# Optimization experiments

Hardware: AMD Instinct MI355X
Metric: run time of the kernel (lower is better)

The kernel has to match this reference:

```python
import jax, jax.numpy as jnp
import numpy as np
import math

DIM = 4096
N_HEADS = 32
HEAD_DIM = DIM // N_HEADS  # 128
SEQLEN = 2048


def setup_inputs() -> dict:
    key = jax.random.key(0)
    ks = jax.random.split(key, 8)
    x = jax.random.normal(ks[0], (1, SEQLEN, DIM), dtype=jnp.float32)
    # freqs_cis as real view: (seqlen, head_dim//2, 2) = (cos, sin) of rotary angles
    theta = 10000.0 ** (-jnp.arange(0, HEAD_DIM, 2, dtype=jnp.float32) / HEAD_DIM)
    angles = jnp.arange(SEQLEN, dtype=jnp.float32)[:, None] * theta[None, :]
    freqs = jnp.stack([jnp.cos(angles), jnp.sin(angles)], axis=-1)  # (S, 64, 2)
    # causal additive mask (use -1e9 instead of -inf for numeric safety)
    mask = jnp.triu(jnp.full((SEQLEN, SEQLEN), -1e9, dtype=jnp.float32), k=1)[None, None]
    scale = 1.0 / math.sqrt(DIM)
    wq = jax.random.normal(ks[1], (DIM, DIM), dtype=jnp.float32) * scale
    wk = jax.random.normal(ks[2], (DIM, DIM), dtype=jnp.float32) * scale
    wv = jax.random.normal(ks[3], (DIM, DIM), dtype=jnp.float32) * scale
    wo = jax.random.normal(ks[4], (DIM, DIM), dtype=jnp.float32) * scale
    return {"x": x, "start_pos": 0, "freqs": freqs, "mask": mask,
            "wq": wq, "wk": wk, "wv": wv, "wo": wo}


def _rotary(xq, xk, freqs, seqlen, n_heads, head_dim):
    # Faithful to source: note the repo's slice(0, 2) means xq_ == xq (no pair swap).
    ll = freqs[:, :, 0:1]  # (S, hd/2, 1) cos
    rr = freqs[:, :, 1:2]  # (S, hd/2, 1) sin
    fl = jnp.concatenate([ll, ll], axis=-1).reshape(seqlen, 1, head_dim)
    fr = jnp.concatenate([-rr, rr], axis=-1).reshape(seqlen, 1, head_dim)
    xq_ = xq.reshape(seqlen, n_heads, head_dim // 2, 2).reshape(seqlen, n_heads, head_dim)  # == xq
    xk_ = xk.reshape(seqlen, n_heads, head_dim // 2, 2).reshape(seqlen, n_heads, head_dim)  # == xk
    return xq * fl + xq_ * fr, xk * fl + xk_ * fr


def reference(x, start_pos, freqs, mask, wq, wk, wv, wo):
    bsz, seqlen, dim = x.shape  # bsz == 1 (source squeezes batch)
    xs = x[0]  # (S, D) -- HE encrypt/linear/decrypt roundtrip == plain linear
    xq = xs @ wq.T
    xk = xs @ wk.T
    xv = xs @ wv.T
    xq = xq.reshape(seqlen, N_HEADS, HEAD_DIM)
    xk = xk.reshape(seqlen, N_HEADS, HEAD_DIM)
    xv = xv.reshape(seqlen, N_HEADS, HEAD_DIM)
    xq, xk = _rotary(xq, xk, freqs, seqlen, N_HEADS, HEAD_DIM)
    # start_pos == 0 and zero-initialized cache => keys/values are just xk/xv
    q = jnp.transpose(xq, (1, 0, 2))  # (H, S, Dh)
    k = jnp.transpose(xk, (1, 0, 2))
    v = jnp.transpose(xv, (1, 0, 2))
    scores = jnp.einsum('hqd,hkd->hqk', q, k) / math.sqrt(HEAD_DIM)  # (H, S, S)
    scores = scores[None] + mask  # (1, H, S, S)
    probs = jax.nn.softmax(scores, axis=-1)
    out = jnp.einsum('bhqk,hkd->bhqd', probs, v)  # (1, H, S, Dh)
    out = jnp.transpose(out, (0, 2, 1, 3)).reshape(bsz, seqlen, dim)
    return out @ wo.T
```

## Files before the change

### kernel.cpp

```cpp
#include <hip/hip_runtime.h>

#define DIM 4096
#define SEQ 2048
#define NH 32
#define HD 128

typedef __bf16 bf16x8 __attribute__((ext_vector_type(8)));
typedef float f32x4 __attribute__((ext_vector_type(4)));

#define QSCALE 0.12751649736765598f

__device__ inline ushort f2bf(float f) {
    union { float f; unsigned u; } v; v.f = f;
    unsigned r = v.u + 0x7fffu + ((v.u >> 16) & 1u);
    return (ushort)(r >> 16);
}

__global__ void conv_all(const float* __restrict__ x,  const float* __restrict__ wq,
                         const float* __restrict__ wk, const float* __restrict__ wv,
                         const float* __restrict__ wo,
                         ushort* __restrict__ xb,  ushort* __restrict__ wqb,
                         ushort* __restrict__ wkb, ushort* __restrict__ wvb,
                         ushort* __restrict__ wob) {
    int i = blockIdx.x * 256 + threadIdx.x;
    const float* src; ushort* dst; int off;
    const int n4x = (SEQ * DIM) / 4;
    if (i < n4x) { src = x; dst = xb; off = i; }
    else {
        int j = i - n4x;
        int w = j >> 22;
        off = j & ((1 << 22) - 1);
        src = (w == 0) ? wq : (w == 1) ? wk : (w == 2) ? wv : wo;
        dst = (w == 0) ? wqb : (w == 1) ? wkb : (w == 2) ? wvb : wob;
    }
    float4 v = ((const float4*)src)[off];
    ushort4 o;
    o.x = f2bf(v.x); o.y = f2bf(v.y); o.z = f2bf(v.z); o.w = f2bf(v.w);
    ((ushort4*)dst)[off] = o;
}

__global__ __launch_bounds__(256)
void gemm_qkv(const ushort* __restrict__ A,
              const ushort* __restrict__ Bq, const ushort* __restrict__ Bk,
              const ushort* __restrict__ Bv,
              ushort* __restrict__ qout, ushort* __restrict__ kout,
              ushort* __restrict__ vt, const float* __restrict__ freqs) {
    __shared__ __align__(16) ushort sA[128 * 64];
    __shared__ __align__(16) ushort sB[128 * 64];
    const int bi = blockIdx.x;
    const int x = bi & 7;
    const int l = bi >> 3;
    const int mblk = l & 15;
    const int nblk = x * 12 + (l >> 4);
    const int wsel = nblk >> 5;
    const int nloc = (nblk & 31) * 128;
    const int m0 = mblk * 128;
    const int tid = threadIdx.x;
    const int wave = tid >> 6, lane = tid & 63;
    const int quad = lane >> 4, c = lane & 15;
    const int wm = (wave >> 1) * 64, wn = (wave & 1) * 64;
    const ushort* B = (wsel == 0) ? Bq : (wsel == 1) ? Bk : Bv;
    const int K = DIM;

    const f32x4 vzero = {0.f, 0.f, 0.f, 0.f};
    f32x4 acc[4][4];
#pragma unroll
    for (int i = 0; i < 4; i++)
#pragma unroll
        for (int j = 0; j < 4; j++) acc[i][j] = vzero;

    const int srow8 = lane >> 3;
    const int sg    = (lane & 7) ^ srow8;
    const int scol  = sg * 8;
    const int rp0 = ((0 * 4 + quad) ^ (c & 7)) * 8;
    const int rp1 = ((1 * 4 + quad) ^ (c & 7)) * 8;
    const size_t arow0 = (size_t)(m0 + wave * 32) * K;
    const size_t brow0 = (size_t)(nloc + wave * 32) * K;

    for (int k0 = 0; k0 < K; k0 += 64) {
#pragma unroll
        for (int i = 0; i < 4; i++) {
            __builtin_amdgcn_global_load_lds(
                (const __attribute__((address_space(1))) void*)(A + arow0 + (size_t)(i * 8 + srow8) * K + k0 + scol),
                (__attribute__((address_space(3))) void*)(&sA[(wave * 32 + i * 8) * 64]), 16, 0, 0);
            __builtin_amdgcn_global_load_lds(
                (const __attribute__((address_space(1))) void*)(B + brow0 + (size_t)(i * 8 + srow8) * K + k0 + scol),
                (__attribute__((address_space(3))) void*)(&sB[(wave * 32 + i * 8) * 64]), 16, 0, 0);
        }
        __syncthreads();
#pragma unroll
        for (int kk = 0; kk < 2; kk++) {
            const int rp = kk ? rp1 : rp0;
            bf16x8 af[4], bfr[4];
#pragma unroll
            for (int t = 0; t < 4; t++) {
                af[t]  = *(const bf16x8*)&sA[(wm + t * 16 + c) * 64 + rp];
                bfr[t] = *(const bf16x8*)&sB[(wn + t * 16 + c) * 64 + rp];
            }
#pragma unroll
            for (int mt = 0; mt < 4; mt++)
#pragma unroll
                for (int nt = 0; nt < 4; nt++)
                    acc[mt][nt] = __builtin_amdgcn_mfma_f32_16x16x32_bf16(af[mt], bfr[nt], acc[mt][nt], 0, 0, 0);
        }
        __syncthreads();
    }

    if (wsel < 2) {
        ushort* Cw = wsel ? kout : qout;
        const float qs = wsel ? 1.0f : QSCALE;
#pragma unroll
        for (int mt = 0; mt < 4; mt++) {
#pragma unroll
            for (int nt = 0; nt < 4; nt++) {
                int colg = nloc + wn + nt * 16 + c;
                int dh = (colg & 127) >> 1;
#pragma unroll
                for (int r = 0; r < 4; r++) {
                    int row = m0 + wm + mt * 16 + quad * 4 + r;
                    float2 f2 = ((const float2*)freqs)[row * 64 + dh];
                    float f = (f2.x + ((c & 1) ? f2.y : -f2.y)) * qs;
                    Cw[(size_t)row * DIM + colg] = f2bf(acc[mt][nt][r] * f);
                }
            }
        }
    } else {
#pragma unroll
        for (int mt = 0; mt < 4; mt++) {
#pragma unroll
            for (int nt = 0; nt < 4; nt++) {
                int cv = nloc + wn + nt * 16 + c;
                int row0 = m0 + wm + mt * 16 + quad * 4;
                ushort4 o;
                o.x = f2bf(acc[mt][nt][0]); o.y = f2bf(acc[mt][nt][1]);
                o.z = f2bf(acc[mt][nt][2]); o.w = f2bf(acc[mt][nt][3]);
                *(ushort4*)&vt[(size_t)cv * SEQ + row0] = o;
            }
        }
    }
}

__global__ __launch_bounds__(256)
void gemm_f32out(const ushort* __restrict__ A, const ushort* __restrict__ B,
                 float* __restrict__ C, int M, int N, int K) {
    __shared__ __align__(16) ushort sA[128 * 64];
    __shared__ __align__(16) ushort sB[128 * 64];
    const int bi = blockIdx.x;
    const int x = bi & 7;
    const int l = bi >> 3;
    const int mblk = l & 15;
    const int nblk = x * 4 + (l >> 4);
    const int m0 = mblk * 128, n0 = nblk * 128;
    const int tid = threadIdx.x;
    const int wave = tid >> 6, lane = tid & 63;
    const int quad = lane >> 4, c = lane & 15;
    const int wm = (wave >> 1) * 64, wn = (wave & 1) * 64;

    const f32x4 vzero = {0.f, 0.f, 0.f, 0.f};
    f32x4 acc[4][4];
#pragma unroll
    for (int i = 0; i < 4; i++)
#pragma unroll
        for (int j = 0; j < 4; j++) acc[i][j] = vzero;

    const int srow8 = lane >> 3;
    const int sg    = (lane & 7) ^ srow8;
    const int scol  = sg * 8;
    const int rp0 = ((0 * 4 + quad) ^ (c & 7)) * 8;
    const int rp1 = ((1 * 4 + quad) ^ (c & 7)) * 8;
    const size_t arow0 = (size_t)(m0 + wave * 32) * K;
    const size_t brow0 = (size_t)(n0 + wave * 32) * K;

    for (int k0 = 0; k0 < K; k0 += 64) {
#pragma unroll
        for (int i = 0; i < 4; i++) {
            __builtin_amdgcn_global_load_lds(
                (const __attribute__((address_space(1))) void*)(A + arow0 + (size_t)(i * 8 + srow8) * K + k0 + scol),
                (__attribute__((address_space(3))) void*)(&sA[(wave * 32 + i * 8) * 64]), 16, 0, 0);
            __builtin_amdgcn_global_load_lds(
                (const __attribute__((address_space(1))) void*)(B + brow0 + (size_t)(i * 8 + srow8) * K + k0 + scol),
                (__attribute__((address_space(3))) void*)(&sB[(wave * 32 + i * 8) * 64]), 16, 0, 0);
        }
        __syncthreads();
#pragma unroll
        for (int kk = 0; kk < 2; kk++) {
            const int rp = kk ? rp1 : rp0;
            bf16x8 af[4], bfr[4];
#pragma unroll
            for (int t = 0; t < 4; t++) {
                af[t]  = *(const bf16x8*)&sA[(wm + t * 16 + c) * 64 + rp];
                bfr[t] = *(const bf16x8*)&sB[(wn + t * 16 + c) * 64 + rp];
            }
#pragma unroll
            for (int mt = 0; mt < 4; mt++)
#pragma unroll
                for (int nt = 0; nt < 4; nt++)
                    acc[mt][nt] = __builtin_amdgcn_mfma_f32_16x16x32_bf16(af[mt], bfr[nt], acc[mt][nt], 0, 0, 0);
        }
        __syncthreads();
    }

#pragma unroll
    for (int mt = 0; mt < 4; mt++)
#pragma unroll
        for (int nt = 0; nt < 4; nt++)
#pragma unroll
            for (int r = 0; r < 4; r++) {
                int row = m0 + wm + mt * 16 + quad * 4 + r;
                int col = n0 + wn + nt * 16 + c;
                C[(size_t)row * N + col] = acc[mt][nt][r];
            }
}

__global__ __launch_bounds__(256)
void flash_kernel(const ushort* __restrict__ Q, const ushort* __restrict__ K,
                  const ushort* __restrict__ Vt, ushort* __restrict__ O) {
    const int bi = blockIdx.x;
    const int h = bi & (NH - 1);
    const int p = bi >> 5;
    __shared__ __align__(16) ushort sK[64 * 128];
    __shared__ __align__(16) ushort sVt[128 * 64];
    __shared__ __align__(16) ushort sP[4][16 * 72];
    const int tid = threadIdx.x, wave = tid >> 6, lane = tid & 63;
    const int quad = lane >> 4, c = lane & 15;

    for (int pass = 0; pass < 2; pass++) {
        const int qb = pass ? (SEQ / 64 - 1 - p) : p;
        const int q0 = qb * 64;

        bf16x8 qf[4];
        {
            const ushort* Qp = Q + (size_t)(q0 + wave * 16 + c) * DIM + h * HD;
#pragma unroll
            for (int ks = 0; ks < 4; ks++) qf[ks] = *(const bf16x8*)(Qp + ks * 32 + quad * 8);
        }
        const f32x4 vzero = {0.f, 0.f, 0.f, 0.f};
        f32x4 oa[8];
#pragma unroll
        for (int dt = 0; dt < 8; dt++) oa[dt] = vzero;
        float ms[4], ls[4];
#pragma unroll
        for (int r = 0; r < 4; r++) { ms[r] = -1e30f; ls[r] = 0.f; }

        for (int kt = 0; kt <= qb; kt++) {
            __syncthreads();
#pragma unroll
            for (int i = 0; i < 4; i++) {
                int lr = wave * 16 + i * 4 + (lane >> 4);
                int ch = lane & 15;
                int g = (ch & 8) | ((ch ^ lr) & 7);
                __builtin_amdgcn_global_load_lds(
                    (const __attribute__((address_space(1))) void*)(K + (size_t)(kt * 64 + lr) * DIM + h * HD + g * 8),
                    (__attribute__((address_space(3))) void*)(&sK[(wave * 16 + i * 4) * 128]), 16, 0, 0);
            }
#pragma unroll
            for (int i = 0; i < 4; i++) {
                int ld = wave * 32 + i * 8 + (lane >> 3);
                int ch = lane & 7;
                int g = (ch ^ ld) & 7;
                __builtin_amdgcn_global_load_lds(
                    (const __attribute__((address_space(1))) void*)(Vt + (size_t)(h * HD + ld) * SEQ + kt * 64 + g * 8),
                    (__attribute__((address_space(3))) void*)(&sVt[(wave * 32 + i * 8) * 64]), 16, 0, 0);
            }
            __syncthreads();

            f32x4 s[4];
#pragma unroll
            for (int nt = 0; nt < 4; nt++) s[nt] = vzero;
#pragma unroll
            for (int ks = 0; ks < 4; ks++)
#pragma unroll
                for (int nt = 0; nt < 4; nt++) {
                    int lr = nt * 16 + c;
                    int gc = ks * 4 + quad;
                    int pch = (gc & 8) | ((gc ^ lr) & 7);
                    bf16x8 kf = *(const bf16x8*)&sK[lr * 128 + pch * 8];
                    s[nt] = __builtin_amdgcn_mfma_f32_16x16x32_bf16(qf[ks], kf, s[nt], 0, 0, 0);
                }

            if (kt == qb) {
#pragma unroll
                for (int nt = 0; nt < 4; nt++)
#pragma unroll
                    for (int r = 0; r < 4; r++) {
                        int keyg = nt * 16 + c;
                        int qg   = wave * 16 + quad * 4 + r;
                        if (keyg > qg) s[nt][r] = -1e30f;
                    }
            }

            float mnew[4], alpha[4];
#pragma unroll
            for (int r = 0; r < 4; r++) {
                float v = fmaxf(fmaxf(s[0][r], s[1][r]), fmaxf(s[2][r], s[3][r]));
                v = fmaxf(v, __shfl_xor(v, 1));
                v = fmaxf(v, __shfl_xor(v, 2));
                v = fmaxf(v, __shfl_xor(v, 4));
                v = fmaxf(v, __shfl_xor(v, 8));
                mnew[r]  = fmaxf(ms[r], v);
                alpha[r] = exp2f(ms[r] - mnew[r]);
                ms[r]    = mnew[r];
            }
            float rs[4] = {0.f, 0.f, 0.f, 0.f};
#pragma unroll
            for (int nt = 0; nt < 4; nt++)
#pragma unroll
                for (int r = 0; r < 4; r++) {
                    float pv = exp2f(s[nt][r] - mnew[r]);
                    rs[r] += pv;
                    sP[wave][(quad * 4 + r) * 72 + nt * 16 + c] = f2bf(pv);
                }
#pragma unroll
            for (int r = 0; r < 4; r++) {
                float v = rs[r];
                v += __shfl_xor(v, 1);
                v += __shfl_xor(v, 2);
                v += __shfl_xor(v, 4);
                v += __shfl_xor(v, 8);
                ls[r] = ls[r] * alpha[r] + v;
            }
#pragma unroll
            for (int dt = 0; dt < 8; dt++)
#pragma unroll
                for (int r = 0; r < 4; r++) oa[dt][r] *= alpha[r];

            __asm__ volatile("s_waitcnt lgkmcnt(0)" ::: "memory");

#pragma unroll
            for (int k2 = 0; k2 < 2; k2++) {
                bf16x8 pf = *(const bf16x8*)&sP[wave][c * 72 + k2 * 32 + quad * 8];
#pragma unroll
                for (int dt = 0; dt < 8; dt++) {
                    int ld = dt * 16 + c;
                    int gc = k2 * 4 + quad;
                    int pch = (gc ^ ld) & 7;
                    bf16x8 vf = *(const bf16x8*)&sVt[ld * 64 + pch * 8];
                    oa[dt] = __builtin_amdgcn_mfma_f32_16x16x32_bf16(pf, vf, oa[dt], 0, 0, 0);
                }
            }
        }

#pragma unroll
        for (int r = 0; r < 4; r++) {
            float inv = 1.f / ls[r];
            int row = q0 + wave * 16 + quad * 4 + r;
#pragma unroll
            for (int dt = 0; dt < 8; dt++)
                O[(size_t)row * DIM + h * HD + dt * 16 + c] = f2bf(oa[dt][r] * inv);
        }
    }
}

extern "C" void kernel_launch(void* const* d_in, const int* in_sizes, int n_in,
                              void* d_out, int out_size, void* d_ws, size_t ws_size,
                              hipStream_t stream) {
    const float* x     = (const float*)d_in[0];
    const float* freqs = (const float*)d_in[2];
    const float* wq    = (const float*)d_in[4];
    const float* wk    = (const float*)d_in[5];
    const float* wv    = (const float*)d_in[6];
    const float* wo    = (const float*)d_in[7];
    float* out = (float*)d_out;

    ushort* xb    = (ushort*)d_ws;
    ushort* wqb   = xb    + (size_t)SEQ * DIM;
    ushort* wkb   = wqb   + (size_t)DIM * DIM;
    ushort* wvb   = wkb   + (size_t)DIM * DIM;
    ushort* wob   = wvb   + (size_t)DIM * DIM;
    ushort* qbuf  = wob   + (size_t)DIM * DIM;
    ushort* kbuf  = qbuf  + (size_t)SEQ * DIM;
    ushort* vtbuf = kbuf  + (size_t)SEQ * DIM;
    ushort* obuf  = vtbuf + (size_t)SEQ * DIM;

    const int n4tot = (SEQ * DIM + 4 * DIM * DIM) / 4;
    conv_all<<<n4tot / 256, 256, 0, stream>>>(x, wq, wk, wv, wo, xb, wqb, wkb, wvb, wob);

    gemm_qkv<<<dim3(3 * DIM / 128 * SEQ / 128), 256, 0, stream>>>(
        xb, wqb, wkb, wvb, qbuf, kbuf, vtbuf, freqs);

    flash_kernel<<<dim3(NH * SEQ / 128), 256, 0, stream>>>(qbuf, kbuf, vtbuf, obuf);

    gemm_f32out<<<dim3(DIM / 128 * SEQ / 128), 256, 0, stream>>>(obuf, wob, out, SEQ, DIM, DIM);
}
```

Baseline: 769.7 us.

## Use 256x256 double-buffered pipelined GEMM tiles for QKV and output projections

```diff
diff --git a/kernel.cpp b/kernel.cpp
--- a/kernel.cpp
+++ b/kernel.cpp
@@ -39,176 +39,236 @@
     ((ushort4*)dst)[off] = o;
 }
 
-__global__ __launch_bounds__(256)
+
+#define AS1(p) (const __attribute__((address_space(1))) void*)(p)
+#define AS3(p) (__attribute__((address_space(3))) void*)(p)
+#define FENCE() asm volatile("" ::: "memory")
+#define BARRIER() do { FENCE(); __builtin_amdgcn_sched_barrier(0); \
+    __builtin_amdgcn_s_barrier(); \
+    __builtin_amdgcn_sched_barrier(0); FENCE(); } while (0)
+#define LGKM0() do { asm volatile("s_waitcnt lgkmcnt(0)" ::: "memory"); \
+    __builtin_amdgcn_sched_barrier(0); } while (0)
+
+__device__ __forceinline__ void gemm256_body(
+    const ushort* __restrict__ Ab,
+    const ushort* __restrict__ Bb,
+    ushort* __restrict__ sA0, ushort* __restrict__ sA1,
+    ushort* __restrict__ sB0, ushort* __restrict__ sB1,
+    f32x4 acc[8][4], const int K)
+{
+    const int tid  = threadIdx.x;
+    const int wave = tid >> 6, lane = tid & 63;
+    const int quad = lane >> 4, c = lane & 15;
+    const int wm = wave >> 2, wn = wave & 3;
+
+    const int aoff = (lane >> 3) * K + (((lane & 7) ^ (lane >> 3)) * 8);
+    const int sa_r0 = wave * 8;
+    const int sb_r0 = (wave >> 1) * 64 + (wave & 1) * 16;
+
+    const int rp0 = ((0 * 4 + quad) ^ (c & 7)) * 8;
+    const int rp1 = ((1 * 4 + quad) ^ (c & 7)) * 8;
+    const int arow = (wm * 128 + c) * 64;
+    const int brow = (wn * 64 + c) * 64;
+
+#define STAGE_A(dst, h, k0) do { \
+    const int _r0 = (h) * 64 + sa_r0; \
+    __builtin_amdgcn_global_load_lds(AS1(Ab + (size_t)_r0 * K + (k0) + aoff), \
+                                     AS3((dst) + _r0 * 64), 16, 0, 0); \
+    const int _r1 = _r0 + 128; \
+    __builtin_amdgcn_global_load_lds(AS1(Ab + (size_t)_r1 * K + (k0) + aoff), \
+                                     AS3((dst) + _r1 * 64), 16, 0, 0); \
+  } while (0)
+#define STAGE_B(dst, h, k0) do { \
+    const int _r0 = (h) * 32 + sb_r0; \
+    __builtin_amdgcn_global_load_lds(AS1(Bb + (size_t)_r0 * K + (k0) + aoff), \
+                                     AS3((dst) + _r0 * 64), 16, 0, 0); \
+    const int _r1 = _r0 + 8; \
+    __builtin_amdgcn_global_load_lds(AS1(Bb + (size_t)_r1 * K + (k0) + aoff), \
+                                     AS3((dst) + _r1 * 64), 16, 0, 0); \
+  } while (0)
+
+    bf16x8 af[4][2], bfr[2][2];
+
+#define READ_AH(buf, mh) do { \
+    _Pragma("unroll") \
+    for (int mt = 0; mt < 4; ++mt) { \
+        af[mt][0] = *(const bf16x8*)&(buf)[arow + (mh) * 4096 + mt * 1024 + rp0]; \
+        af[mt][1] = *(const bf16x8*)&(buf)[arow + (mh) * 4096 + mt * 1024 + rp1]; \
+    } } while (0)
+#define READ_BH(buf, nh) do { \
+    _Pragma("unroll") \
+    for (int nt = 0; nt < 2; ++nt) { \
+        bfr[nt][0] = *(const bf16x8*)&(buf)[brow + (nh) * 2048 + nt * 1024 + rp0]; \
+        bfr[nt][1] = *(const bf16x8*)&(buf)[brow + (nh) * 2048 + nt * 1024 + rp1]; \
+    } } while (0)
+#define MMA_Q(mh, nh) do { \
+    __builtin_amdgcn_s_setprio(1); \
+    _Pragma("unroll") \
+    for (int kk = 0; kk < 2; ++kk) \
+    _Pragma("unroll") \
+    for (int mt = 0; mt < 4; ++mt) \
+    _Pragma("unroll") \
+    for (int nt = 0; nt < 2; ++nt) \
+        acc[(mh)*4+mt][(nh)*2+nt] = __builtin_amdgcn_mfma_f32_16x16x32_bf16( \
+            af[mt][kk], bfr[nt][kk], acc[(mh)*4+mt][(nh)*2+nt], 0, 0, 0); \
+    __builtin_amdgcn_s_setprio(0); \
+  } while (0)
+
+    const int NT = K >> 6;
+
+    STAGE_A(sA0, 0, 0);  STAGE_B(sB0, 0, 0);
+    STAGE_A(sA0, 1, 0);  STAGE_B(sB0, 1, 0);
+    STAGE_A(sA1, 0, 64); STAGE_B(sB1, 0, 64);
+    asm volatile("s_waitcnt vmcnt(4)" ::: "memory");
+    BARRIER();
+
+    for (int t = 0; t < NT; ++t) {
+        ushort* cA = (t & 1) ? sA1 : sA0;
+        ushort* cB = (t & 1) ? sB1 : sB0;
+        ushort* nA = (t & 1) ? sA0 : sA1;
+        ushort* nB = (t & 1) ? sB0 : sB1;
+        const int kn  = (t + 1) << 6;
+        const int kn2 = (t + 2) << 6;
+        const bool ok1 = (t + 1 < NT), ok2 = (t + 2 < NT);
+
+        READ_AH(cA, 0); READ_BH(cB, 0);
+        if (ok1) STAGE_A(nA, 1, kn);
+        BARRIER(); LGKM0();
+        MMA_Q(0, 0);
+        BARRIER();
+
+        READ_BH(cB, 1);
+        if (ok1) STAGE_B(nB, 1, kn);
+        BARRIER(); LGKM0();
+        MMA_Q(0, 1);
+        BARRIER();
+
+        READ_AH(cA, 1); READ_BH(cB, 0);
+        if (ok2) STAGE_A(cA, 0, kn2);
+        BARRIER(); LGKM0();
+        MMA_Q(1, 0);
+        BARRIER();
+
+        READ_BH(cB, 1);
+        if (ok2) STAGE_B(cB, 0, kn2);
+        BARRIER(); LGKM0();
+        MMA_Q(1, 1);
+        if (t < NT - 1) {
+            if (ok2) asm volatile("s_waitcnt vmcnt(4)" ::: "memory");
+            else     asm volatile("s_waitcnt vmcnt(0)" ::: "memory");
+        }
+        BARRIER();
+    }
+#undef STAGE_A
+#undef STAGE_B
+#undef READ_AH
+#undef READ_BH
+#undef MMA_Q
+}
+
+__global__ __launch_bounds__(512, 2)
 void gemm_qkv(const ushort* __restrict__ A,
               const ushort* __restrict__ Bq, const ushort* __restrict__ Bk,
               const ushort* __restrict__ Bv,
               ushort* __restrict__ qout, ushort* __restrict__ kout,
               ushort* __restrict__ vt, const float* __restrict__ freqs) {
-    __shared__ __align__(16) ushort sA[128 * 64];
-    __shared__ __align__(16) ushort sB[128 * 64];
+    __shared__ __align__(16) ushort sA[2][256 * 64];
+    __shared__ __align__(16) ushort sB[2][256 * 64];
     const int bi = blockIdx.x;
     const int x = bi & 7;
     const int l = bi >> 3;
-    const int mblk = l & 15;
-    const int nblk = x * 12 + (l >> 4);
-    const int wsel = nblk >> 5;
-    const int nloc = (nblk & 31) * 128;
-    const int m0 = mblk * 128;
+    const int mblk = l & 7;
+    const int nblk = x * 6 + (l >> 3);
+    const int wsel = nblk >> 4;
+    const int nloc = (nblk & 15) * 256;
+    const int m0 = mblk * 256;
+    const ushort* B = (wsel == 0) ? Bq : (wsel == 1) ? Bk : Bv;
+
+    const f32x4 vzero = {0.f, 0.f, 0.f, 0.f};
+    f32x4 acc[8][4];
+#pragma unroll
+    for (int i = 0; i < 8; i++)
+#pragma unroll
+        for (int j = 0; j < 4; j++) acc[i][j] = vzero;
+
+    gemm256_body(A + (size_t)m0 * DIM, B + (size_t)nloc * DIM,
+                 &sA[0][0], &sA[1][0], &sB[0][0], &sB[1][0], acc, DIM);
+
     const int tid = threadIdx.x;
     const int wave = tid >> 6, lane = tid & 63;
     const int quad = lane >> 4, c = lane & 15;
-    const int wm = (wave >> 1) * 64, wn = (wave & 1) * 64;
-    const ushort* B = (wsel == 0) ? Bq : (wsel == 1) ? Bk : Bv;
-    const int K = DIM;
-
-    const f32x4 vzero = {0.f, 0.f, 0.f, 0.f};
-    f32x4 acc[4][4];
-#pragma unroll
-    for (int i = 0; i < 4; i++)
-#pragma unroll
-        for (int j = 0; j < 4; j++) acc[i][j] = vzero;
-
-    const int srow8 = lane >> 3;
-    const int sg    = (lane & 7) ^ srow8;
-    const int scol  = sg * 8;
-    const int rp0 = ((0 * 4 + quad) ^ (c & 7)) * 8;
-    const int rp1 = ((1 * 4 + quad) ^ (c & 7)) * 8;
-    const size_t arow0 = (size_t)(m0 + wave * 32) * K;
-    const size_t brow0 = (size_t)(nloc + wave * 32) * K;
-
-    for (int k0 = 0; k0 < K; k0 += 64) {
-#pragma unroll
-        for (int i = 0; i < 4; i++) {
-            __builtin_amdgcn_global_load_lds(
-                (const __attribute__((address_space(1))) void*)(A + arow0 + (size_t)(i * 8 + srow8) * K + k0 + scol),
-                (__attribute__((address_space(3))) void*)(&sA[(wave * 32 + i * 8) * 64]), 16, 0, 0);
-            __builtin_amdgcn_global_load_lds(
-                (const __attribute__((address_space(1))) void*)(B + brow0 + (size_t)(i * 8 + srow8) * K + k0 + scol),
-                (__attribute__((address_space(3))) void*)(&sB[(wave * 32 + i * 8) * 64]), 16, 0, 0);
-        }
-        __syncthreads();
-#pragma unroll
-        for (int kk = 0; kk < 2; kk++) {
-            const int rp = kk ? rp1 : rp0;
-            bf16x8 af[4], bfr[4];
-#pragma unroll
-            for (int t = 0; t < 4; t++) {
-                af[t]  = *(const bf16x8*)&sA[(wm + t * 16 + c) * 64 + rp];
-                bfr[t] = *(const bf16x8*)&sB[(wn + t * 16 + c) * 64 + rp];
-            }
-#pragma unroll
-            for (int mt = 0; mt < 4; mt++)
-#pragma unroll
-                for (int nt = 0; nt < 4; nt++)
-                    acc[mt][nt] = __builtin_amdgcn_mfma_f32_16x16x32_bf16(af[mt], bfr[nt], acc[mt][nt], 0, 0, 0);
-        }
-        __syncthreads();
-    }
+    const int wm = wave >> 2, wn = wave & 3;
 
     if (wsel < 2) {
         ushort* Cw = wsel ? kout : qout;
         const float qs = wsel ? 1.0f : QSCALE;
 #pragma unroll
-        for (int mt = 0; mt < 4; mt++) {
-#pragma unroll
-            for (int nt = 0; nt < 4; nt++) {
-                int colg = nloc + wn + nt * 16 + c;
+        for (int i = 0; i < 8; i++) {
+#pragma unroll
+            for (int j = 0; j < 4; j++) {
+                int colg = nloc + wn * 64 + j * 16 + c;
                 int dh = (colg & 127) >> 1;
 #pragma unroll
                 for (int r = 0; r < 4; r++) {
-                    int row = m0 + wm + mt * 16 + quad * 4 + r;
+                    int row = m0 + wm * 128 + i * 16 + quad * 4 + r;
                     float2 f2 = ((const float2*)freqs)[row * 64 + dh];
                     float f = (f2.x + ((c & 1) ? f2.y : -f2.y)) * qs;
-                    Cw[(size_t)row * DIM + colg] = f2bf(acc[mt][nt][r] * f);
+                    Cw[(size_t)row * DIM + colg] = f2bf(acc[i][j][r] * f);
                 }
             }
         }
     } else {
 #pragma unroll
-        for (int mt = 0; mt < 4; mt++) {
-#pragma unroll
-            for (int nt = 0; nt < 4; nt++) {
-                int cv = nloc + wn + nt * 16 + c;
-                int row0 = m0 + wm + mt * 16 + quad * 4;
+        for (int i = 0; i < 8; i++) {
+#pragma unroll
+            for (int j = 0; j < 4; j++) {
+                int cv = nloc + wn * 64 + j * 16 + c;
+                int row0 = m0 + wm * 128 + i * 16 + quad * 4;
                 ushort4 o;
-                o.x = f2bf(acc[mt][nt][0]); o.y = f2bf(acc[mt][nt][1]);
-                o.z = f2bf(acc[mt][nt][2]); o.w = f2bf(acc[mt][nt][3]);
+                o.x = f2bf(acc[i][j][0]); o.y = f2bf(acc[i][j][1]);
+                o.z = f2bf(acc[i][j][2]); o.w = f2bf(acc[i][j][3]);
                 *(ushort4*)&vt[(size_t)cv * SEQ + row0] = o;
             }
         }
     }
 }
 
-__global__ __launch_bounds__(256)
+__global__ __launch_bounds__(512, 2)
 void gemm_f32out(const ushort* __restrict__ A, const ushort* __restrict__ B,
                  float* __restrict__ C, int M, int N, int K) {
-    __shared__ __align__(16) ushort sA[128 * 64];
-    __shared__ __align__(16) ushort sB[128 * 64];
+    __shared__ __align__(16) ushort sA[2][256 * 64];
+    __shared__ __align__(16) ushort sB[2][256 * 64];
     const int bi = blockIdx.x;
     const int x = bi & 7;
     const int l = bi >> 3;
-    const int mblk = l & 15;
-    const int nblk = x * 4 + (l >> 4);
-    const int m0 = mblk * 128, n0 = nblk * 128;
+    const int mblk = l & 7;
+    const int nblk = x * 2 + (l >> 3);
+    const int m0 = mblk * 256, n0 = nblk * 256;
+
+    const f32x4 vzero = {0.f, 0.f, 0.f, 0.f};
+    f32x4 acc[8][4];
+#pragma unroll
+    for (int i = 0; i < 8; i++)
+#pragma unroll
+        for (int j = 0; j < 4; j++) acc[i][j] = vzero;
+
+    gemm256_body(A + (size_t)m0 * K, B + (size_t)n0 * K,
+                 &sA[0][0], &sA[1][0], &sB[0][0], &sB[1][0], acc, K);
+
     const int tid = threadIdx.x;
     const int wave = tid >> 6, lane = tid & 63;
     const int quad = lane >> 4, c = lane & 15;
-    const int wm = (wave >> 1) * 64, wn = (wave & 1) * 64;
-
-    const f32x4 vzero = {0.f, 0.f, 0.f, 0.f};
-    f32x4 acc[4][4];
-#pragma unroll
-    for (int i = 0; i < 4; i++)
-#pragma unroll
-        for (int j = 0; j < 4; j++) acc[i][j] = vzero;
-
-    const int srow8 = lane >> 3;
-    const int sg    = (lane & 7) ^ srow8;
-    const int scol  = sg * 8;
-    const int rp0 = ((0 * 4 + quad) ^ (c & 7)) * 8;
-    const int rp1 = ((1 * 4 + quad) ^ (c & 7)) * 8;
-    const size_t arow0 = (size_t)(m0 + wave * 32) * K;
-    const size_t brow0 = (size_t)(n0 + wave * 32) * K;
-
-    for (int k0 = 0; k0 < K; k0 += 64) {
-#pragma unroll
-        for (int i = 0; i < 4; i++) {
-            __builtin_amdgcn_global_load_lds(
-                (const __attribute__((address_space(1))) void*)(A + arow0 + (size_t)(i * 8 + srow8) * K + k0 + scol),
-                (__attribute__((address_space(3))) void*)(&sA[(wave * 32 + i * 8) * 64]), 16, 0, 0);
-            __builtin_amdgcn_global_load_lds(
-                (const __attribute__((address_space(1))) void*)(B + brow0 + (size_t)(i * 8 + srow8) * K + k0 + scol),
-                (__attribute__((address_space(3))) void*)(&sB[(wave * 32 + i * 8) * 64]), 16, 0, 0);
-        }
-        __syncthreads();
-#pragma unroll
-        for (int kk = 0; kk < 2; kk++) {
-            const int rp = kk ? rp1 : rp0;
-            bf16x8 af[4], bfr[4];
-#pragma unroll
-            for (int t = 0; t < 4; t++) {
-                af[t]  = *(const bf16x8*)&sA[(wm + t * 16 + c) * 64 + rp];
-                bfr[t] = *(const bf16x8*)&sB[(wn + t * 16 + c) * 64 + rp];
-            }
-#pragma unroll
-            for (int mt = 0; mt < 4; mt++)
-#pragma unroll
-                for (int nt = 0; nt < 4; nt++)
-                    acc[mt][nt] = __builtin_amdgcn_mfma_f32_16x16x32_bf16(af[mt], bfr[nt], acc[mt][nt], 0, 0, 0);
-        }
-        __syncthreads();
-    }
-
-#pragma unroll
-    for (int mt = 0; mt < 4; mt++)
-#pragma unroll
-        for (int nt = 0; nt < 4; nt++)
+    const int wm = wave >> 2, wn = wave & 3;
+
+#pragma unroll
+    for (int i = 0; i < 8; i++)
+#pragma unroll
+        for (int j = 0; j < 4; j++)
 #pragma unroll
             for (int r = 0; r < 4; r++) {
-                int row = m0 + wm + mt * 16 + quad * 4 + r;
-                int col = n0 + wn + nt * 16 + c;
-                C[(size_t)row * N + col] = acc[mt][nt][r];
+                int row = m0 + wm * 128 + i * 16 + quad * 4 + r;
+                int col = n0 + wn * 64 + j * 16 + c;
+                C[(size_t)row * N + col] = acc[i][j][r];
             }
 }
 
@@ -375,10 +435,9 @@
     const int n4tot = (SEQ * DIM + 4 * DIM * DIM) / 4;
     conv_all<<<n4tot / 256, 256, 0, stream>>>(x, wq, wk, wv, wo, xb, wqb, wkb, wvb, wob);
 
-    gemm_qkv<<<dim3(3 * DIM / 128 * SEQ / 128), 256, 0, stream>>>(
-        xb, wqb, wkb, wvb, qbuf, kbuf, vtbuf, freqs);
+    gemm_qkv<<<dim3(384), 512, 0, stream>>>(xb, wqb, wkb, wvb, qbuf, kbuf, vtbuf, freqs);
 
     flash_kernel<<<dim3(NH * SEQ / 128), 256, 0, stream>>>(qbuf, kbuf, vtbuf, obuf);
 
-    gemm_f32out<<<dim3(DIM / 128 * SEQ / 128), 256, 0, stream>>>(obuf, wob, out, SEQ, DIM, DIM);
-}
+    gemm_f32out<<<dim3(128), 512, 0, stream>>>(obuf, wob, out, SEQ, DIM, DIM);
+}
```

After: 749.0 us. 1.03x faster.
